# Optimization experiments

Hardware: AMD Instinct MI355X
Metric: run time of the kernel (lower is better)

The kernel has to match this reference:

```python
import jax, jax.numpy as jnp
import numpy as np
from jax import lax

DIM = 256
D_STATE = 16
SPARSITY = 0.3


def setup_inputs() -> dict:
    key = jax.random.key(0)
    ks = jax.random.split(key, 12)
    B, L, C = 16, 8192, DIM
    x = jax.random.normal(ks[0], (B, L, C), dtype=jnp.float32)
    # DyT params
    alpha = jnp.ones((1,), jnp.float32) * 0.5
    dyt_w = jnp.ones((C,), jnp.float32) + 0.02 * jax.random.normal(ks[1], (C,))
    dyt_b = 0.02 * jax.random.normal(ks[2], (C,))
    # proj_in / proj_out (torch Linear: y = x @ W.T + b)
    s = 1.0 / np.sqrt(C)
    Wi = jax.random.uniform(ks[3], (C, C), minval=-s, maxval=s)
    bi = jax.random.uniform(ks[4], (C,), minval=-s, maxval=s)
    Wo = jax.random.uniform(ks[5], (C, C), minval=-s, maxval=s)
    bo = jax.random.uniform(ks[6], (C,), minval=-s, maxval=s)
    # depthwise kernel_size=1 conv -> per-channel scale
    conv_w = jax.random.uniform(ks[7], (C,), minval=-1.0, maxval=1.0)
    # SSM params (nn.Parameter zeros in source; use small random for a meaningful test)
    A = 0.02 * jax.random.normal(ks[8], (D_STATE, D_STATE))
    Bp = 0.02 * jax.random.normal(ks[9], (1, 1, D_STATE))
    Cp = 0.02 * jax.random.normal(ks[10], (C, D_STATE))
    return {"x": x, "alpha": alpha, "dyt_w": dyt_w, "dyt_b": dyt_b,
            "Wi": Wi, "bi": bi, "conv_w": conv_w,
            "A": A, "Bp": Bp, "Cp": Cp, "Wo": Wo, "bo": bo}


def reference(x, alpha, dyt_w, dyt_b, Wi, bi, conv_w, A, Bp, Cp, Wo, bo):
    B, L, C = x.shape
    residual = x
    # DyT norm
    x_norm = jnp.tanh(alpha * x) * dyt_w + dyt_b
    # proj_in
    x_proj = x_norm @ Wi.T + bi                      # [B, L, C]
    # cosine similarity to center token, softmax over L
    center = x_proj[:, L // 2]                        # [B, C]
    eps = 1e-12
    xpn = x_proj / jnp.maximum(jnp.linalg.norm(x_proj, axis=-1, keepdims=True), eps)
    cn = center / jnp.maximum(jnp.linalg.norm(center, axis=-1, keepdims=True), eps)
    sim = jax.nn.softmax(jnp.einsum('blc,bc->bl', xpn, cn), axis=-1)  # [B, L]
    k = max(1, int(L * SPARSITY))
    _, topk_idx = lax.top_k(sim, k)                   # [B, k]
    # gather selected tokens
    x_sparse = jnp.take_along_axis(x_proj, topk_idx[:, :, None], axis=1)  # [B, k, C]
    # depthwise kernel-1 conv == per-channel scale
    x_conv = x_sparse * conv_w                        # [B, k, C]
    # SSM scan: h_{t} = h_{t-1} @ A.T + sigmoid(B) * x_t;  y_t = sum(h * sigmoid(C))
    sB = jax.nn.sigmoid(Bp)                           # [1, 1, d_state]
    sC = jax.nn.sigmoid(Cp)                           # [C, d_state]

    def step(h, xt):
        # h: [B, C, d_state], xt: [B, C]
        h = h @ A.T + sB * xt[:, :, None]
        y = jnp.sum(h * sC, axis=-1)                  # [B, C]
        return h, y

    h0 = jnp.zeros((B, C, D_STATE), x.dtype)
    _, ys = lax.scan(step, h0, jnp.swapaxes(x_conv, 0, 1))  # ys: [k, B, C]
    x_processed = jnp.swapaxes(ys, 0, 1) @ Wo.T + bo        # [B, k, C]
    # scatter back to full sequence (topk indices are unique per row)
    out = jnp.zeros_like(x).at[jnp.arange(B)[:, None], topk_idx].set(x_processed)
    return out + residual, sim
```

## Files before the change

kernel.cpp:

```cpp
#include <hip/hip_runtime.h>
#include <math.h>

#define B_ 16
#define L_ 8192
#define C_ 256
#define KTOP 2457
#define JT 20
#define M1 (B_*L_)
#define M2 (B_*KTOP)

#define XP_OFF  ((size_t)0)
#define Y_OFF   (XP_OFF + (size_t)M1*C_)
#define CN_OFF  (Y_OFF  + (size_t)M2*C_)
#define CF_OFF  (CN_OFF + (size_t)B_*C_)
#define IDX_OFF (CF_OFF + (size_t)JT*C_)
#define WIT_OFF (IDX_OFF + (size_t)M2)
#define WOT_OFF (WIT_OFF + (size_t)C_*C_)

__global__ __launch_bounds__(256) void prep_kernel(
    const float* __restrict__ Wi, const float* __restrict__ Wo,
    float* __restrict__ WiT, float* __restrict__ WoT,
    const float* __restrict__ A, const float* __restrict__ Bp, const float* __restrict__ Cp,
    float* __restrict__ cf,
    const float* __restrict__ x, const float* __restrict__ bi, const float* __restrict__ alpha,
    const float* __restrict__ dw, const float* __restrict__ db, float* __restrict__ cn)
{
    __shared__ float shm[1089];
    const int bid = blockIdx.x, tid = threadIdx.x;
    if (bid < 128) {
        const int z = bid >> 6, rem = bid & 63;
        const int r0 = (rem >> 3) * 32, c0 = (rem & 7) * 32;
        const float* src = z ? Wo : Wi;
        float* dst = z ? WoT : WiT;
        float (*t)[33] = (float(*)[33])shm;
        int tx = tid & 31, ty = tid >> 5;
        #pragma unroll
        for (int r = 0; r < 4; r++)
            t[ty + r*8][tx] = src[(size_t)(r0 + ty + r*8)*C_ + c0 + tx];
        __syncthreads();
        #pragma unroll
        for (int r = 0; r < 4; r++)
            dst[(size_t)(c0 + ty + r*8)*C_ + r0 + tx] = t[tx][ty + r*8];
    } else if (bid == 128) {
        int c = tid;
        float* As = shm;
        float* v0 = shm + 256;
        As[c] = A[c];
        if (c < 16) v0[c] = 1.0f / (1.0f + expf(-Bp[c]));
        float sC[16];
        #pragma unroll
        for (int i = 0; i < 16; i++) sC[i] = 1.0f / (1.0f + expf(-Cp[c*16 + i]));
        __syncthreads();
        float v[16];
        #pragma unroll
        for (int i = 0; i < 16; i++) v[i] = v0[i];
        for (int j = 0; j < JT; j++) {
            float d = 0.f;
            #pragma unroll
            for (int i = 0; i < 16; i++) d += sC[i] * v[i];
            cf[j*C_ + c] = d;
            float nv[16];
            #pragma unroll
            for (int i = 0; i < 16; i++) {
                float s = 0.f;
                #pragma unroll
                for (int m = 0; m < 16; m++) s += As[i*16 + m] * v[m];
                nv[i] = s;
            }
            #pragma unroll
            for (int i = 0; i < 16; i++) v[i] = nv[i];
        }
    } else {
        int b = bid - 129, c = tid;
        float* xn = shm;
        float* red = shm + 256;
        float al = alpha[0];
        size_t base = ((size_t)b*L_ + L_/2)*C_;
        xn[c] = tanhf(al*x[base + c])*dw[c] + db[c];
        __syncthreads();
        float s = bi[c];
        #pragma unroll 8
        for (int k = 0; k < 256; k++) s = fmaf(xn[k], Wi[(size_t)c*C_ + k], s);
        float ss = s*s;
        #pragma unroll
        for (int off = 32; off; off >>= 1) ss += __shfl_xor(ss, off);
        if ((c & 63) == 0) red[c >> 6] = ss;
        __syncthreads();
        float tot = red[0] + red[1] + red[2] + red[3];
        float inv = 1.0f / fmaxf(sqrtf(tot), 1e-12f);
        cn[b*C_ + c] = s * inv;
    }
}

__global__ __launch_bounds__(256, 2) void gemm1_kernel(
    const float* __restrict__ x, const float* __restrict__ WiT,
    const float* __restrict__ bi, const float* __restrict__ alpha,
    const float* __restrict__ dw, const float* __restrict__ db,
    const float* __restrict__ cn, float* __restrict__ xp,
    float* __restrict__ dtp, float* __restrict__ ssp)
{
    __shared__ float As[2][32*132];
    __shared__ float Bs[2][32*128];
    const int tid = threadIdx.x;
    const int tm2 = tid >> 4;
    const int tn2 = tid & 15;
    const int m0 = blockIdx.x * 128;
    const int n0 = blockIdx.y * 128;
    const int b  = m0 >> 13;
    const float al = alpha[0];

    float acc[8][8];
    #pragma unroll
    for (int i = 0; i < 8; i++)
        #pragma unroll
        for (int j = 0; j < 8; j++) acc[i][j] = 0.f;

    float4 xa[4], wv[4];
    #pragma unroll
    for (int it = 0; it < 4; it++) {
        int i2 = tid + it*256;
        xa[it] = *(const float4*)&x[(size_t)(m0 + (i2>>3))*C_ + ((i2&7)*4)];
        wv[it] = *(const float4*)&WiT[(size_t)(i2>>5)*C_ + n0 + ((i2&31)*4)];
    }
    #pragma unroll
    for (int it = 0; it < 4; it++) {
        int i2 = tid + it*256;
        int ar = i2>>3, ak = (i2&7)*4;
        float4 v = xa[it];
        float4 w = *(const float4*)&dw[ak];
        float4 bb = *(const float4*)&db[ak];
        As[0][(ak+0)*132 + ar] = tanhf(al*v.x)*w.x + bb.x;
        As[0][(ak+1)*132 + ar] = tanhf(al*v.y)*w.y + bb.y;
        As[0][(ak+2)*132 + ar] = tanhf(al*v.z)*w.z + bb.z;
        As[0][(ak+3)*132 + ar] = tanhf(al*v.w)*w.w + bb.w;
        *(float4*)&Bs[0][(i2>>5)*128 + (i2&31)*4] = wv[it];
    }
    __syncthreads();
    int cur = 0;
    for (int k0 = 0; k0 < C_; k0 += 32) {
        if (k0 + 32 < C_) {
            #pragma unroll
            for (int it = 0; it < 4; it++) {
                int i2 = tid + it*256;
                xa[it] = *(const float4*)&x[(size_t)(m0 + (i2>>3))*C_ + k0 + 32 + ((i2&7)*4)];
                wv[it] = *(const float4*)&WiT[(size_t)(k0 + 32 + (i2>>5))*C_ + n0 + ((i2&31)*4)];
            }
        }
        #pragma unroll 2
        for (int kk = 0; kk < 32; kk++) {
            float a[8], bf[8];
            *(float4*)&a[0]  = *(const float4*)&As[cur][kk*132 + tm2*8];
            *(float4*)&a[4]  = *(const float4*)&As[cur][kk*132 + tm2*8 + 4];
            *(float4*)&bf[0] = *(const float4*)&Bs[cur][kk*128 + tn2*4];
            *(float4*)&bf[4] = *(const float4*)&Bs[cur][kk*128 + tn2*4 + 64];
            #pragma unroll
            for (int i = 0; i < 8; i++)
                #pragma unroll
                for (int j = 0; j < 8; j++)
                    acc[i][j] = fmaf(a[i], bf[j], acc[i][j]);
        }
        if (k0 + 32 < C_) {
            int nxt = cur ^ 1;
            #pragma unroll
            for (int it = 0; it < 4; it++) {
                int i2 = tid + it*256;
                int ar = i2>>3, ak = (i2&7)*4;
                float4 v = xa[it];
                float4 w = *(const float4*)&dw[k0 + 32 + ak];
                float4 bb = *(const float4*)&db[k0 + 32 + ak];
                As[nxt][(ak+0)*132 + ar] = tanhf(al*v.x)*w.x + bb.x;
                As[nxt][(ak+1)*132 + ar] = tanhf(al*v.y)*w.y + bb.y;
                As[nxt][(ak+2)*132 + ar] = tanhf(al*v.z)*w.z + bb.z;
                As[nxt][(ak+3)*132 + ar] = tanhf(al*v.w)*w.w + bb.w;
                *(float4*)&Bs[nxt][(i2>>5)*128 + (i2&31)*4] = wv[it];
            }
            cur = nxt;
        }
        __syncthreads();
    }
    float4 bi0 = *(const float4*)&bi[n0 + tn2*4];
    float4 bi1 = *(const float4*)&bi[n0 + 64 + tn2*4];
    float4 c0  = *(const float4*)&cn[b*C_ + n0 + tn2*4];
    float4 c1  = *(const float4*)&cn[b*C_ + n0 + 64 + tn2*4];
    #pragma unroll
    for (int i = 0; i < 8; i++) {
        size_t row = m0 + tm2*8 + i;
        float4 o0 = make_float4(acc[i][0]+bi0.x, acc[i][1]+bi0.y, acc[i][2]+bi0.z, acc[i][3]+bi0.w);
        float4 o1 = make_float4(acc[i][4]+bi1.x, acc[i][5]+bi1.y, acc[i][6]+bi1.z, acc[i][7]+bi1.w);
        *(float4*)&xp[row*C_ + n0 + tn2*4]      = o0;
        *(float4*)&xp[row*C_ + n0 + 64 + tn2*4] = o1;
        float dt = o0.x*c0.x + o0.y*c0.y + o0.z*c0.z + o0.w*c0.w
                 + o1.x*c1.x + o1.y*c1.y + o1.z*c1.z + o1.w*c1.w;
        float ss = o0.x*o0.x + o0.y*o0.y + o0.z*o0.z + o0.w*o0.w
                 + o1.x*o1.x + o1.y*o1.y + o1.z*o1.z + o1.w*o1.w;
        #pragma unroll
        for (int off = 8; off; off >>= 1) {
            dt += __shfl_xor(dt, off);
            ss += __shfl_xor(ss, off);
        }
        if (tn2 == 0) {
            dtp[(size_t)blockIdx.y*M1 + row] = dt;
            ssp[(size_t)blockIdx.y*M1 + row] = ss;
        }
    }
}

__global__ __launch_bounds__(1024) void softmax_kernel(
    const float* __restrict__ dtp, const float* __restrict__ ssp,
    float* __restrict__ sim, unsigned long long* __restrict__ kw)
{
    __shared__ float scratch[32];
    const int b = blockIdx.x, tid = threadIdx.x;
    const int lane = tid & 63, wid = tid >> 6;
    float ev[8];
    #pragma unroll
    for (int s = 0; s < 8; s++) {
        size_t m = (size_t)b*L_ + tid + s*1024;
        float dt = dtp[m] + dtp[M1 + m];
        float ssv = ssp[m] + ssp[M1 + m];
        ev[s] = dt / fmaxf(sqrtf(ssv), 1e-12f);
    }
    float mx = ev[0];
    #pragma unroll
    for (int s = 1; s < 8; s++) mx = fmaxf(mx, ev[s]);
    #pragma unroll
    for (int off = 32; off; off >>= 1) mx = fmaxf(mx, __shfl_xor(mx, off));
    if (lane == 0) scratch[wid] = mx;
    __syncthreads();
    if (tid == 0) {
        float m2 = scratch[0];
        for (int i = 1; i < 16; i++) m2 = fmaxf(m2, scratch[i]);
        scratch[20] = m2;
    }
    __syncthreads();
    mx = scratch[20];
    float pv[8], sum = 0.f;
    #pragma unroll
    for (int s = 0; s < 8; s++) { pv[s] = expf(ev[s] - mx); sum += pv[s]; }
    #pragma unroll
    for (int off = 32; off; off >>= 1) sum += __shfl_xor(sum, off);
    __syncthreads();
    if (lane == 0) scratch[wid] = sum;
    __syncthreads();
    if (tid == 0) {
        float s2 = 0.f;
        for (int i = 0; i < 16; i++) s2 += scratch[i];
        scratch[21] = s2;
    }
    __syncthreads();
    float inv = 1.0f / scratch[21];
    #pragma unroll
    for (int s = 0; s < 8; s++) {
        int l = tid + s*1024;
        float sm = pv[s] * inv;
        sim[(size_t)b*L_ + l] = sm;
        kw[(size_t)b*L_ + l] =
            ((unsigned long long)__float_as_uint(sm) << 32) | (unsigned)(0xFFFFFFFFu - l);
    }
}

__global__ __launch_bounds__(256) void sort1k_kernel(unsigned long long* __restrict__ keys)
{
    __shared__ unsigned long long k[1024];
    size_t base = (size_t)blockIdx.x * 1024;
    int tid = threadIdx.x;
    #pragma unroll
    for (int s = 0; s < 4; s++) k[tid + s*256] = keys[base + tid + s*256];
    __syncthreads();
    for (int ksz = 2; ksz <= 1024; ksz <<= 1) {
        for (int j = ksz >> 1; j > 0; j >>= 1) {
            #pragma unroll
            for (int s = 0; s < 2; s++) {
                int p = tid + s*256;
                int i = ((p & ~(j-1)) << 1) | (p & (j-1));
                int ix = i | j;
                unsigned long long a = k[i], c = k[ix];
                bool desc = ((i & ksz) == 0);
                if (desc ? (a < c) : (a > c)) { k[i] = c; k[ix] = a; }
            }
            __syncthreads();
        }
    }
    #pragma unroll
    for (int s = 0; s < 4; s++) keys[base + tid + s*256] = k[tid + s*256];
}

#define MT 2048
__global__ __launch_bounds__(256) void merge_kernel(
    const unsigned long long* __restrict__ src, unsigned long long* __restrict__ dst, int run)
{
    const size_t tile = blockIdx.x;
    const size_t pairSpan = (size_t)2 * run;
    const size_t p = tile * MT / pairSpan;
    const int o = (int)(tile * MT % pairSpan);
    const unsigned long long* A  = src + p * pairSpan;
    const unsigned long long* Bv = A + run;
    unsigned long long* D = dst + p * pairSpan;

    int q0 = o + threadIdx.x * (MT/256);
    int lo = (q0 > run) ? (q0 - run) : 0;
    int hi = (q0 < run) ? q0 : run;
    while (lo < hi) {
        int mid = (lo + hi) >> 1;
        if (A[mid] >= Bv[q0 - 1 - mid]) lo = mid + 1; else hi = mid;
    }
    int a = lo, bq = q0 - lo;
    #pragma unroll
    for (int q = 0; q < MT/256; q++) {
        unsigned long long va = (a < run) ? A[a] : 0ULL;
        unsigned long long vb = (bq < run) ? Bv[bq] : 0ULL;
        bool takeA = (bq >= run) || ((a < run) && (va > vb));
        D[q0 + q] = takeA ? va : vb;
        if (takeA) a++; else bq++;
    }
}

__global__ __launch_bounds__(256) void merge_top_kernel(
    const unsigned long long* __restrict__ src, int* __restrict__ idxo)
{
    const int tile = blockIdx.x;
    const int p = tile >> 1;
    const int o = (tile & 1) * MT;
    const int run = 4096;
    const unsigned long long* A  = src + (size_t)p * L_;
    const unsigned long long* Bv = A + run;

    int q0 = o + threadIdx.x * (MT/256);
    int lo = (q0 > run) ? (q0 - run) : 0;
    int hi = (q0 < run) ? q0 : run;
    while (lo < hi) {
        int mid = (lo + hi) >> 1;
        if (A[mid] >= Bv[q0 - 1 - mid]) lo = mid + 1; else hi = mid;
    }
    int a = lo, bq = q0 - lo;
    #pragma unroll
    for (int q = 0; q < MT/256; q++) {
        unsigned long long va = (a < run) ? A[a] : 0ULL;
        unsigned long long vb = (bq < run) ? Bv[bq] : 0ULL;
        bool takeA = (bq >= run) || ((a < run) && (va > vb));
        unsigned long long v = takeA ? va : vb;
        if (q0 + q < KTOP)
            idxo[p*KTOP + q0 + q] = (int)(0xFFFFFFFFu - (unsigned)(v & 0xFFFFFFFFu));
        if (takeA) a++; else bq++;
    }
}

#define TT 32
__global__ __launch_bounds__(256) void y_kernel(const float* __restrict__ xp,
    const int* __restrict__ idx, const float* __restrict__ conv_w,
    const float* __restrict__ cf, float* __restrict__ y)
{
    __shared__ float rows[(TT + JT - 1) * C_];
    const int b = blockIdx.y;
    const int t0 = blockIdx.x * TT;
    const int tid = threadIdx.x;
    const int c4 = (tid & 63) * 4;
    const int tg = tid >> 6;
    const int* idxb = idx + b*KTOP;

    for (int s = tid; s < (TT + JT - 1) * 64; s += 256) {
        int r = s >> 6, cq = (s & 63) * 4;
        int gi = t0 - (JT - 1) + r;
        float4 v = make_float4(0.f, 0.f, 0.f, 0.f);
        if (gi >= 0 && gi < KTOP) {
            int l = idxb[gi];
            v = *(const float4*)&xp[((size_t)b*L_ + l)*C_ + cq];
        }
        *(float4*)&rows[r*C_ + cq] = v;
    }
    float4 cfr[JT];
    #pragma unroll
    for (int j = 0; j < JT; j++) cfr[j] = *(const float4*)&cf[j*C_ + c4];
    float4 cw = *(const float4*)&conv_w[c4];
    __syncthreads();

    #pragma unroll
    for (int u = 0; u < TT/4; u++) {
        int tl = tg + u*4;
        int t = t0 + tl;
        if (t < KTOP) {
            float4 acc = make_float4(0.f, 0.f, 0.f, 0.f);
            #pragma unroll
            for (int j = 0; j < JT; j++) {
                const float4 v = *(const float4*)&rows[(tl + JT - 1 - j)*C_ + c4];
                acc.x = fmaf(cfr[j].x, v.x, acc.x);
                acc.y = fmaf(cfr[j].y, v.y, acc.y);
                acc.z = fmaf(cfr[j].z, v.z, acc.z);
                acc.w = fmaf(cfr[j].w, v.w, acc.w);
            }
            acc.x *= cw.x; acc.y *= cw.y; acc.z *= cw.z; acc.w *= cw.w;
            *(float4*)&y[((size_t)b*KTOP + t)*C_ + c4] = acc;
        }
    }
}

__global__ void copy_kernel(const float4* __restrict__ src, float4* __restrict__ dst)
{
    size_t n4 = (size_t)M1*C_/4;
    for (size_t i = (size_t)blockIdx.x*blockDim.x + threadIdx.x; i < n4;
         i += (size_t)gridDim.x*blockDim.x)
        dst[i] = src[i];
}

__global__ __launch_bounds__(256, 2) void gemm2_kernel(
    const float* __restrict__ y, const float* __restrict__ WoT,
    const float* __restrict__ bo, const float* __restrict__ x,
    const int* __restrict__ idx, float* __restrict__ out0)
{
    __shared__ float As[2][32*132];
    __shared__ float Bs[2][32*128];
    const int tid = threadIdx.x;
    const int tm2 = tid >> 4;
    const int tn2 = tid & 15;
    const int m0 = blockIdx.x * 128;
    const int n0 = blockIdx.y * 128;

    float acc[8][8];
    #pragma unroll
    for (int i = 0; i < 8; i++)
        #pragma unroll
        for (int j = 0; j < 8; j++) acc[i][j] = 0.f;

    float4 xa[4], wv[4];
    #pragma unroll
    for (int it = 0; it < 4; it++) {
        int i2 = tid + it*256;
        int m = m0 + (i2>>3);
        xa[it] = (m < M2) ? *(const float4*)&y[(size_t)m*C_ + ((i2&7)*4)]
                          : make_float4(0.f, 0.f, 0.f, 0.f);
        wv[it] = *(const float4*)&WoT[(size_t)(i2>>5)*C_ + n0 + ((i2&31)*4)];
    }
    #pragma unroll
    for (int it = 0; it < 4; it++) {
        int i2 = tid + it*256;
        int ar = i2>>3, ak = (i2&7)*4;
        float4 v = xa[it];
        As[0][(ak+0)*132 + ar] = v.x;
        As[0][(ak+1)*132 + ar] = v.y;
        As[0][(ak+2)*132 + ar] = v.z;
        As[0][(ak+3)*132 + ar] = v.w;
        *(float4*)&Bs[0][(i2>>5)*128 + (i2&31)*4] = wv[it];
    }
    __syncthreads();
    int cur = 0;
    for (int k0 = 0; k0 < C_; k0 += 32) {
        if (k0 + 32 < C_) {
            #pragma unroll
            for (int it = 0; it < 4; it++) {
                int i2 = tid + it*256;
                int m = m0 + (i2>>3);
                xa[it] = (m < M2) ? *(const float4*)&y[(size_t)m*C_ + k0 + 32 + ((i2&7)*4)]
                                  : make_float4(0.f, 0.f, 0.f, 0.f);
                wv[it] = *(const float4*)&WoT[(size_t)(k0 + 32 + (i2>>5))*C_ + n0 + ((i2&31)*4)];
            }
        }
        #pragma unroll 2
        for (int kk = 0; kk < 32; kk++) {
            float a[8], bf[8];
            *(float4*)&a[0]  = *(const float4*)&As[cur][kk*132 + tm2*8];
            *(float4*)&a[4]  = *(const float4*)&As[cur][kk*132 + tm2*8 + 4];
            *(float4*)&bf[0] = *(const float4*)&Bs[cur][kk*128 + tn2*4];
            *(float4*)&bf[4] = *(const float4*)&Bs[cur][kk*128 + tn2*4 + 64];
            #pragma unroll
            for (int i = 0; i < 8; i++)
                #pragma unroll
                for (int j = 0; j < 8; j++)
                    acc[i][j] = fmaf(a[i], bf[j], acc[i][j]);
        }
        if (k0 + 32 < C_) {
            int nxt = cur ^ 1;
            #pragma unroll
            for (int it = 0; it < 4; it++) {
                int i2 = tid + it*256;
                int ar = i2>>3, ak = (i2&7)*4;
                float4 v = xa[it];
                As[nxt][(ak+0)*132 + ar] = v.x;
                As[nxt][(ak+1)*132 + ar] = v.y;
                As[nxt][(ak+2)*132 + ar] = v.z;
                As[nxt][(ak+3)*132 + ar] = v.w;
                *(float4*)&Bs[nxt][(i2>>5)*128 + (i2&31)*4] = wv[it];
            }
            cur = nxt;
        }
        __syncthreads();
    }
    float4 bo0 = *(const float4*)&bo[n0 + tn2*4];
    float4 bo1 = *(const float4*)&bo[n0 + 64 + tn2*4];
    #pragma unroll
    for (int i = 0; i < 8; i++) {
        int m = m0 + tm2*8 + i;
        if (m < M2) {
            int b = m / KTOP, t = m - b*KTOP;
            int l = idx[b*KTOP + t];
            size_t base = ((size_t)b*L_ + l)*C_;
            float4 x0 = *(const float4*)&x[base + n0 + tn2*4];
            float4 x1 = *(const float4*)&x[base + n0 + 64 + tn2*4];
            float4 o0 = make_float4(acc[i][0]+bo0.x+x0.x, acc[i][1]+bo0.y+x0.y,
                                    acc[i][2]+bo0.z+x0.z, acc[i][3]+bo0.w+x0.w);
            float4 o1 = make_float4(acc[i][4]+bo1.x+x1.x, acc[i][5]+bo1.y+x1.y,
                                    acc[i][6]+bo1.z+x1.z, acc[i][7]+bo1.w+x1.w);
            *(float4*)&out0[base + n0 + tn2*4]      = o0;
            *(float4*)&out0[base + n0 + 64 + tn2*4] = o1;
        }
    }
}

extern "C" void kernel_launch(void* const* d_in, const int* in_sizes, int n_in,
                              void* d_out, int out_size, void* d_ws, size_t ws_size,
                              hipStream_t stream)
{
    const float* x      = (const float*)d_in[0];
    const float* alpha  = (const float*)d_in[1];
    const float* dyt_w  = (const float*)d_in[2];
    const float* dyt_b  = (const float*)d_in[3];
    const float* Wi     = (const float*)d_in[4];
    const float* bi     = (const float*)d_in[5];
    const float* conv_w = (const float*)d_in[6];
    const float* A      = (const float*)d_in[7];
    const float* Bp     = (const float*)d_in[8];
    const float* Cp     = (const float*)d_in[9];
    const float* Wo     = (const float*)d_in[10];
    const float* bo     = (const float*)d_in[11];

    float* ws  = (float*)d_ws;
    float* xp  = ws + XP_OFF;
    float* yb  = ws + Y_OFF;
    float* cn  = ws + CN_OFF;
    float* cf  = ws + CF_OFF;
    int*   idx = (int*)(ws + IDX_OFF);
    float* WiT = ws + WIT_OFF;
    float* WoT = ws + WOT_OFF;
    unsigned long long* kw1 = (unsigned long long*)(ws + Y_OFF);
    unsigned long long* kw2 = kw1 + (size_t)B_*L_;
    float* dtp = ws + Y_OFF + 524288;
    float* ssp = dtp + (size_t)2*M1;

    float* out0 = (float*)d_out;
    float* sim  = out0 + (size_t)M1*C_;

    prep_kernel<<<145, 256, 0, stream>>>(Wi, Wo, WiT, WoT, A, Bp, Cp, cf,
                                         x, bi, alpha, dyt_w, dyt_b, cn);
    gemm1_kernel<<<dim3(M1/128, 2), 256, 0, stream>>>(x, WiT, bi, alpha, dyt_w, dyt_b,
                                                      cn, xp, dtp, ssp);
    softmax_kernel<<<B_, 1024, 0, stream>>>(dtp, ssp, sim, kw1);
    sort1k_kernel<<<B_*L_/1024, 256, 0, stream>>>(kw1);
    merge_kernel<<<B_*L_/MT, 256, 0, stream>>>(kw1, kw2, 1024);
    merge_kernel<<<B_*L_/MT, 256, 0, stream>>>(kw2, kw1, 2048);
    merge_top_kernel<<<B_*2, 256, 0, stream>>>(kw1, idx);
    y_kernel<<<dim3((KTOP + TT - 1)/TT, B_), 256, 0, stream>>>(xp, idx, conv_w, cf, yb);
    copy_kernel<<<2048, 256, 0, stream>>>((const float4*)x, (float4*)out0);
    gemm2_kernel<<<dim3((M2 + 127)/128, 2), 256, 0, stream>>>(yb, WoT, bo, x, idx, out0);
}
```

Before: 523.5 us.

## Widen gemm1 tile to full N, fuse cosine normalize, async-load weights to LDS

```diff
diff --git a/kernel.cpp b/kernel.cpp
--- a/kernel.cpp
+++ b/kernel.cpp
@@ -16,6 +16,12 @@
 #define IDX_OFF (CF_OFF + (size_t)JT*C_)
 #define WIT_OFF (IDX_OFF + (size_t)M2)
 #define WOT_OFF (WIT_OFF + (size_t)C_*C_)
+
+__device__ __forceinline__ void async_copy16(const float* g, float* l) {
+    __builtin_amdgcn_global_load_lds(
+        (const __attribute__((address_space(1))) void*)g,
+        (__attribute__((address_space(3))) void*)l, 16, 0, 0);
+}
 
 __global__ __launch_bounds__(256) void prep_kernel(
     const float* __restrict__ Wi, const float* __restrict__ Wo,
@@ -96,130 +102,102 @@
     const float* __restrict__ x, const float* __restrict__ WiT,
     const float* __restrict__ bi, const float* __restrict__ alpha,
     const float* __restrict__ dw, const float* __restrict__ db,
-    const float* __restrict__ cn, float* __restrict__ xp,
-    float* __restrict__ dtp, float* __restrict__ ssp)
-{
-    __shared__ float As[2][32*132];
-    __shared__ float Bs[2][32*128];
+    const float* __restrict__ cn, float* __restrict__ xp, float* __restrict__ e)
+{
+    __shared__ float As[32*132];
+    __shared__ float Bs[32*256];
     const int tid = threadIdx.x;
-    const int tm2 = tid >> 4;
-    const int tn2 = tid & 15;
+    const int lane = tid & 63;
+    const int wv = tid >> 6;
+    const int tn2 = tid & 31;
+    const int tm2 = tid >> 5;
     const int m0 = blockIdx.x * 128;
-    const int n0 = blockIdx.y * 128;
     const int b  = m0 >> 13;
     const float al = alpha[0];
 
-    float acc[8][8];
-    #pragma unroll
-    for (int i = 0; i < 8; i++)
+    float acc[16][8];
+    #pragma unroll
+    for (int i = 0; i < 16; i++)
         #pragma unroll
         for (int j = 0; j < 8; j++) acc[i][j] = 0.f;
 
-    float4 xa[4], wv[4];
-    #pragma unroll
-    for (int it = 0; it < 4; it++) {
-        int i2 = tid + it*256;
-        xa[it] = *(const float4*)&x[(size_t)(m0 + (i2>>3))*C_ + ((i2&7)*4)];
-        wv[it] = *(const float4*)&WiT[(size_t)(i2>>5)*C_ + n0 + ((i2&31)*4)];
-    }
-    #pragma unroll
-    for (int it = 0; it < 4; it++) {
-        int i2 = tid + it*256;
-        int ar = i2>>3, ak = (i2&7)*4;
-        float4 v = xa[it];
-        float4 w = *(const float4*)&dw[ak];
-        float4 bb = *(const float4*)&db[ak];
-        As[0][(ak+0)*132 + ar] = tanhf(al*v.x)*w.x + bb.x;
-        As[0][(ak+1)*132 + ar] = tanhf(al*v.y)*w.y + bb.y;
-        As[0][(ak+2)*132 + ar] = tanhf(al*v.z)*w.z + bb.z;
-        As[0][(ak+3)*132 + ar] = tanhf(al*v.w)*w.w + bb.w;
-        *(float4*)&Bs[0][(i2>>5)*128 + (i2&31)*4] = wv[it];
-    }
-    __syncthreads();
-    int cur = 0;
     for (int k0 = 0; k0 < C_; k0 += 32) {
-        if (k0 + 32 < C_) {
-            #pragma unroll
-            for (int it = 0; it < 4; it++) {
-                int i2 = tid + it*256;
-                xa[it] = *(const float4*)&x[(size_t)(m0 + (i2>>3))*C_ + k0 + 32 + ((i2&7)*4)];
-                wv[it] = *(const float4*)&WiT[(size_t)(k0 + 32 + (i2>>5))*C_ + n0 + ((i2&31)*4)];
-            }
-        }
+        #pragma unroll
+        for (int it = 0; it < 8; it++) {
+            int br = wv + it*4;
+            async_copy16(&WiT[(size_t)(k0 + br)*C_ + lane*4], &Bs[br*256]);
+        }
+        #pragma unroll
+        for (int it = 0; it < 4; it++) {
+            int i2 = tid + it*256;
+            int ar = i2 >> 3;
+            int ak = (i2 & 7) * 4;
+            float4 v  = *(const float4*)&x[(size_t)(m0 + ar)*C_ + k0 + ak];
+            float4 w4 = *(const float4*)&dw[k0 + ak];
+            float4 b4 = *(const float4*)&db[k0 + ak];
+            As[(ak+0)*132 + ar] = tanhf(al*v.x)*w4.x + b4.x;
+            As[(ak+1)*132 + ar] = tanhf(al*v.y)*w4.y + b4.y;
+            As[(ak+2)*132 + ar] = tanhf(al*v.z)*w4.z + b4.z;
+            As[(ak+3)*132 + ar] = tanhf(al*v.w)*w4.w + b4.w;
+        }
+        __syncthreads();
         #pragma unroll 2
         for (int kk = 0; kk < 32; kk++) {
-            float a[8], bf[8];
-            *(float4*)&a[0]  = *(const float4*)&As[cur][kk*132 + tm2*8];
-            *(float4*)&a[4]  = *(const float4*)&As[cur][kk*132 + tm2*8 + 4];
-            *(float4*)&bf[0] = *(const float4*)&Bs[cur][kk*128 + tn2*4];
-            *(float4*)&bf[4] = *(const float4*)&Bs[cur][kk*128 + tn2*4 + 64];
-            #pragma unroll
-            for (int i = 0; i < 8; i++)
-                #pragma unroll
-                for (int j = 0; j < 8; j++)
-                    acc[i][j] = fmaf(a[i], bf[j], acc[i][j]);
-        }
-        if (k0 + 32 < C_) {
-            int nxt = cur ^ 1;
-            #pragma unroll
-            for (int it = 0; it < 4; it++) {
-                int i2 = tid + it*256;
-                int ar = i2>>3, ak = (i2&7)*4;
-                float4 v = xa[it];
-                float4 w = *(const float4*)&dw[k0 + 32 + ak];
-                float4 bb = *(const float4*)&db[k0 + 32 + ak];
-                As[nxt][(ak+0)*132 + ar] = tanhf(al*v.x)*w.x + bb.x;
-                As[nxt][(ak+1)*132 + ar] = tanhf(al*v.y)*w.y + bb.y;
-                As[nxt][(ak+2)*132 + ar] = tanhf(al*v.z)*w.z + bb.z;
-                As[nxt][(ak+3)*132 + ar] = tanhf(al*v.w)*w.w + bb.w;
-                *(float4*)&Bs[nxt][(i2>>5)*128 + (i2&31)*4] = wv[it];
-            }
-            cur = nxt;
-        }
-        __syncthreads();
-    }
-    float4 bi0 = *(const float4*)&bi[n0 + tn2*4];
-    float4 bi1 = *(const float4*)&bi[n0 + 64 + tn2*4];
-    float4 c0  = *(const float4*)&cn[b*C_ + n0 + tn2*4];
-    float4 c1  = *(const float4*)&cn[b*C_ + n0 + 64 + tn2*4];
-    #pragma unroll
-    for (int i = 0; i < 8; i++) {
-        size_t row = m0 + tm2*8 + i;
+            float a[16];
+            *(float4*)&a[0]  = *(const float4*)&As[kk*132 + tm2*16];
+            *(float4*)&a[4]  = *(const float4*)&As[kk*132 + tm2*16 + 4];
+            *(float4*)&a[8]  = *(const float4*)&As[kk*132 + tm2*16 + 8];
+            *(float4*)&a[12] = *(const float4*)&As[kk*132 + tm2*16 + 12];
+            float4 b0 = *(const float4*)&Bs[kk*256 + tn2*4];
+            float4 b1 = *(const float4*)&Bs[kk*256 + tn2*4 + 128];
+            #pragma unroll
+            for (int i = 0; i < 16; i++) {
+                acc[i][0] = fmaf(a[i], b0.x, acc[i][0]);
+                acc[i][1] = fmaf(a[i], b0.y, acc[i][1]);
+                acc[i][2] = fmaf(a[i], b0.z, acc[i][2]);
+                acc[i][3] = fmaf(a[i], b0.w, acc[i][3]);
+                acc[i][4] = fmaf(a[i], b1.x, acc[i][4]);
+                acc[i][5] = fmaf(a[i], b1.y, acc[i][5]);
+                acc[i][6] = fmaf(a[i], b1.z, acc[i][6]);
+                acc[i][7] = fmaf(a[i], b1.w, acc[i][7]);
+            }
+        }
+        __syncthreads();
+    }
+    float4 bi0 = *(const float4*)&bi[tn2*4];
+    float4 bi1 = *(const float4*)&bi[tn2*4 + 128];
+    float4 c0  = *(const float4*)&cn[b*C_ + tn2*4];
+    float4 c1  = *(const float4*)&cn[b*C_ + tn2*4 + 128];
+    #pragma unroll
+    for (int i = 0; i < 16; i++) {
+        size_t row = m0 + tm2*16 + i;
         float4 o0 = make_float4(acc[i][0]+bi0.x, acc[i][1]+bi0.y, acc[i][2]+bi0.z, acc[i][3]+bi0.w);
         float4 o1 = make_float4(acc[i][4]+bi1.x, acc[i][5]+bi1.y, acc[i][6]+bi1.z, acc[i][7]+bi1.w);
-        *(float4*)&xp[row*C_ + n0 + tn2*4]      = o0;
-        *(float4*)&xp[row*C_ + n0 + 64 + tn2*4] = o1;
+        *(float4*)&xp[row*C_ + tn2*4]       = o0;
+        *(float4*)&xp[row*C_ + tn2*4 + 128] = o1;
         float dt = o0.x*c0.x + o0.y*c0.y + o0.z*c0.z + o0.w*c0.w
                  + o1.x*c1.x + o1.y*c1.y + o1.z*c1.z + o1.w*c1.w;
         float ss = o0.x*o0.x + o0.y*o0.y + o0.z*o0.z + o0.w*o0.w
                  + o1.x*o1.x + o1.y*o1.y + o1.z*o1.z + o1.w*o1.w;
         #pragma unroll
-        for (int off = 8; off; off >>= 1) {
+        for (int off = 16; off; off >>= 1) {
             dt += __shfl_xor(dt, off);
             ss += __shfl_xor(ss, off);
         }
-        if (tn2 == 0) {
-            dtp[(size_t)blockIdx.y*M1 + row] = dt;
-            ssp[(size_t)blockIdx.y*M1 + row] = ss;
-        }
+        if (tn2 == 0) e[row] = dt / fmaxf(sqrtf(ss), 1e-12f);
     }
 }
 
 __global__ __launch_bounds__(1024) void softmax_kernel(
-    const float* __restrict__ dtp, const float* __restrict__ ssp,
-    float* __restrict__ sim, unsigned long long* __restrict__ kw)
+    const float* __restrict__ e, float* __restrict__ sim, unsigned long long* __restrict__ kw)
 {
     __shared__ float scratch[32];
     const int b = blockIdx.x, tid = threadIdx.x;
     const int lane = tid & 63, wid = tid >> 6;
+    const float* eb = e + (size_t)b*L_;
     float ev[8];
     #pragma unroll
-    for (int s = 0; s < 8; s++) {
-        size_t m = (size_t)b*L_ + tid + s*1024;
-        float dt = dtp[m] + dtp[M1 + m];
-        float ssv = ssp[m] + ssp[M1 + m];
-        ev[s] = dt / fmaxf(sqrtf(ssv), 1e-12f);
-    }
+    for (int s = 0; s < 8; s++) ev[s] = eb[tid + s*1024];
     float mx = ev[0];
     #pragma unroll
     for (int s = 1; s < 8; s++) mx = fmaxf(mx, ev[s]);
@@ -410,6 +388,8 @@
     __shared__ float As[2][32*132];
     __shared__ float Bs[2][32*128];
     const int tid = threadIdx.x;
+    const int lane = tid & 63;
+    const int wv = tid >> 6;
     const int tm2 = tid >> 4;
     const int tn2 = tid & 15;
     const int m0 = blockIdx.x * 128;
@@ -421,14 +401,19 @@
         #pragma unroll
         for (int j = 0; j < 8; j++) acc[i][j] = 0.f;
 
-    float4 xa[4], wv[4];
+    float4 xa[4];
     #pragma unroll
     for (int it = 0; it < 4; it++) {
         int i2 = tid + it*256;
         int m = m0 + (i2>>3);
         xa[it] = (m < M2) ? *(const float4*)&y[(size_t)m*C_ + ((i2&7)*4)]
                           : make_float4(0.f, 0.f, 0.f, 0.f);
-        wv[it] = *(const float4*)&WoT[(size_t)(i2>>5)*C_ + n0 + ((i2&31)*4)];
+    }
+    #pragma unroll
+    for (int it = 0; it < 4; it++) {
+        int brow = 2*wv + it*8;
+        async_copy16(&WoT[(size_t)(brow + (lane>>5))*C_ + n0 + (lane&31)*4],
+                     &Bs[0][brow*128]);
     }
     #pragma unroll
     for (int it = 0; it < 4; it++) {
@@ -439,19 +424,24 @@
         As[0][(ak+1)*132 + ar] = v.y;
         As[0][(ak+2)*132 + ar] = v.z;
         As[0][(ak+3)*132 + ar] = v.w;
-        *(float4*)&Bs[0][(i2>>5)*128 + (i2&31)*4] = wv[it];
     }
     __syncthreads();
     int cur = 0;
     for (int k0 = 0; k0 < C_; k0 += 32) {
         if (k0 + 32 < C_) {
+            int nxt = cur ^ 1;
+            #pragma unroll
+            for (int it = 0; it < 4; it++) {
+                int brow = 2*wv + it*8;
+                async_copy16(&WoT[(size_t)(k0 + 32 + brow + (lane>>5))*C_ + n0 + (lane&31)*4],
+                             &Bs[nxt][brow*128]);
+            }
             #pragma unroll
             for (int it = 0; it < 4; it++) {
                 int i2 = tid + it*256;
                 int m = m0 + (i2>>3);
                 xa[it] = (m < M2) ? *(const float4*)&y[(size_t)m*C_ + k0 + 32 + ((i2&7)*4)]
                                   : make_float4(0.f, 0.f, 0.f, 0.f);
-                wv[it] = *(const float4*)&WoT[(size_t)(k0 + 32 + (i2>>5))*C_ + n0 + ((i2&31)*4)];
             }
         }
         #pragma unroll 2
@@ -478,7 +468,6 @@
                 As[nxt][(ak+1)*132 + ar] = v.y;
                 As[nxt][(ak+2)*132 + ar] = v.z;
                 As[nxt][(ak+3)*132 + ar] = v.w;
-                *(float4*)&Bs[nxt][(i2>>5)*128 + (i2&31)*4] = wv[it];
             }
             cur = nxt;
         }
@@ -532,17 +521,15 @@
     float* WoT = ws + WOT_OFF;
     unsigned long long* kw1 = (unsigned long long*)(ws + Y_OFF);
     unsigned long long* kw2 = kw1 + (size_t)B_*L_;
-    float* dtp = ws + Y_OFF + 524288;
-    float* ssp = dtp + (size_t)2*M1;
+    float* e = ws + Y_OFF + 524288;
 
     float* out0 = (float*)d_out;
     float* sim  = out0 + (size_t)M1*C_;
 
     prep_kernel<<<145, 256, 0, stream>>>(Wi, Wo, WiT, WoT, A, Bp, Cp, cf,
                                          x, bi, alpha, dyt_w, dyt_b, cn);
-    gemm1_kernel<<<dim3(M1/128, 2), 256, 0, stream>>>(x, WiT, bi, alpha, dyt_w, dyt_b,
-                                                      cn, xp, dtp, ssp);
-    softmax_kernel<<<B_, 1024, 0, stream>>>(dtp, ssp, sim, kw1);
+    gemm1_kernel<<<M1/128, 256, 0, stream>>>(x, WiT, bi, alpha, dyt_w, dyt_b, cn, xp, e);
+    softmax_kernel<<<B_, 1024, 0, stream>>>(e, sim, kw1);
     sort1k_kernel<<<B_*L_/1024, 256, 0, stream>>>(kw1);
     merge_kernel<<<B_*L_/MT, 256, 0, stream>>>(kw1, kw2, 1024);
     merge_kernel<<<B_*L_/MT, 256, 0, stream>>>(kw2, kw1, 2048);
```

After: 459.1 us. 1.14x faster.
